# Kernel optimization log

Measured on AMD Instinct MI355X. Metric: run time of the kernel, lower is better.

The kernel has to match this reference:

```python
import jax, jax.numpy as jnp
import numpy as np

NUM_EMBEDDINGS = 512
EMBEDDING_DIM = 64
COMMITMENT_COST = 0.25


def setup_inputs() -> dict:
    key = jax.random.key(0)
    k1, k2 = jax.random.split(key)
    inputs = jax.random.normal(k1, (4, 64, 32, 32, 32), dtype=jnp.float32)
    # torch init: uniform(-1/K, 1/K)
    lim = 1.0 / NUM_EMBEDDINGS
    embedding = jax.random.uniform(k2, (NUM_EMBEDDINGS, EMBEDDING_DIM),
                                   dtype=jnp.float32, minval=-lim, maxval=lim)
    return {"inputs": inputs, "embedding": embedding}


def reference(inputs, embedding):
    # inputs: [B, C, D, H, W] with C == embedding_dim
    x = jnp.transpose(inputs, (0, 2, 3, 4, 1))            # [B,D,H,W,C]
    input_shape = x.shape
    flat = x.reshape(-1, EMBEDDING_DIM)                    # [N,C]
    # squared euclidean distances via matmul expansion
    d = (jnp.sum(flat ** 2, axis=1, keepdims=True)
         + jnp.sum(embedding ** 2, axis=1)
         - 2.0 * flat @ embedding.T)                       # [N,K]
    encoding_indices = jnp.argmin(d, axis=1)               # [N]
    quantized = embedding[encoding_indices].reshape(input_shape)  # [B,D,H,W,C]
    q_latent_loss = jnp.mean((jax.lax.stop_gradient(quantized) - x) ** 2)
    e_latent_loss = jnp.mean((quantized - jax.lax.stop_gradient(x)) ** 2)
    loss = q_latent_loss + COMMITMENT_COST * e_latent_loss
    # straight-through estimator
    quantized = x + jax.lax.stop_gradient(quantized - x)
    quantized = jnp.transpose(quantized, (0, 4, 1, 2, 3))  # [B,C,D,H,W]
    indices = encoding_indices.reshape(input_shape[:-1])   # [B,D,H,W]
    return quantized, loss, indices
```

## Files before the change

kernel.cpp:

```cpp
#include <hip/hip_runtime.h>
#include <math.h>

#define NROWS   131072
#define NCH     64
#define NEMB    512
#define CH_STRIDE 32768
#define B_STRIDE  (64*32768)
#define Q_ELEMS   8388608
#define SPLITS  4
#define KPQ     (NEMB/SPLITS)


__global__ __launch_bounds__(64)
void vq_esq(const float* __restrict__ emb, float* __restrict__ esq) {
    int k = blockIdx.x * 64 + threadIdx.x;
    if (k < NEMB) {
        const float* e = emb + k * NCH;
        float s = 0.f;
        #pragma unroll
        for (int c = 0; c < NCH; ++c) s = fmaf(e[c], e[c], s);
        esq[k] = s;
    }
}

__global__ __launch_bounds__(256, 4)
void vq_scan(const float* __restrict__ in, const float* __restrict__ emb,
             const float* __restrict__ esq,
             unsigned long long* __restrict__ parts) {
    int q      = blockIdx.x & (SPLITS - 1);
    int rowblk = blockIdx.x >> 2;
    int n      = rowblk * 256 + threadIdx.x;
    int b = n >> 15;
    int s = n & 32767;
    const float* xin = in + b * B_STRIDE + s;

    float x[NCH];
    #pragma unroll
    for (int c = 0; c < NCH; ++c) x[c] = xin[c * CH_STRIDE];

    float A;
    {
        float L[16];
        #pragma unroll
        for (int i = 0; i < 16; ++i) {
            float q0 = x[i +  0] * x[i +  0];
            float q1 = x[i + 16] * x[i + 16];
            float q2 = x[i + 32] * x[i + 32];
            float q3 = x[i + 48] * x[i + 48];
            asm volatile("" : "+v"(q0), "+v"(q1), "+v"(q2), "+v"(q3));
            L[i] = (q0 + q1) + (q2 + q3);
        }
        float F[8];
        #pragma unroll
        for (int i = 0; i < 8; ++i) F[i] = L[i] + L[i + 8];
        float G[4];
        #pragma unroll
        for (int i = 0; i < 4; ++i) G[i] = F[i] + F[i + 4];
        A = (G[0] + G[2]) + (G[1] + G[3]);
    }

    int k0 = __builtin_amdgcn_readfirstlane(q * KPQ);
    float m1 = 3.4e38f;
    int   i1 = k0;
    for (int j = 0; j < KPQ; ++j) {
        int k = k0 + j;
        const float* e = emb + k * NCH;
        float acc = 0.f;
        #pragma unroll
        for (int c = 0; c < NCH; ++c) acc = fmaf(x[c], e[c], acc);
        float t1 = A + esq[k];
        float d  = t1 - (acc + acc);
        bool lt = d < m1;
        m1 = lt ? d : m1;
        i1 = lt ? k : i1;
    }

    unsigned long long pk =
        ((unsigned long long)__float_as_uint(m1) << 32) | (unsigned)i1;
    parts[(unsigned)n * SPLITS + q] = pk;
}

__global__ __launch_bounds__(256)
void vq_finish(const float* __restrict__ in, const float* __restrict__ emb,
               const unsigned long long* __restrict__ parts,
               float* __restrict__ out_q, float* __restrict__ out_idx,
               double* __restrict__ loss_acc) {
    int n = blockIdx.x * 256 + threadIdx.x;
    int b = n >> 15;
    int s = n & 32767;

    ulonglong2 pa = *reinterpret_cast<const ulonglong2*>(parts + (unsigned)n * 4);
    ulonglong2 pb = *reinterpret_cast<const ulonglong2*>(parts + (unsigned)n * 4 + 2);
    unsigned long long pk = pa.x;
    if (pa.y < pk) pk = pa.y;
    if (pb.x < pk) pk = pb.x;
    if (pb.y < pk) pk = pb.y;
    int w = (int)(pk & 0xFFFFu);

    const float* xin = in + b * B_STRIDE + s;
    const float* qr  = emb + w * NCH;
    float*       oq  = out_q + b * B_STRIDE + s;
    double rl = 0.0;
    #pragma unroll
    for (int c = 0; c < NCH; c += 4) {
        float4 qv = *reinterpret_cast<const float4*>(qr + c);
        float x0 = xin[(c + 0) * CH_STRIDE];
        float x1 = xin[(c + 1) * CH_STRIDE];
        float x2 = xin[(c + 2) * CH_STRIDE];
        float x3 = xin[(c + 3) * CH_STRIDE];
        oq[(c + 0) * CH_STRIDE] = qv.x;
        oq[(c + 1) * CH_STRIDE] = qv.y;
        oq[(c + 2) * CH_STRIDE] = qv.z;
        oq[(c + 3) * CH_STRIDE] = qv.w;
        double d0 = (double)qv.x - (double)x0;
        double d1 = (double)qv.y - (double)x1;
        double d2 = (double)qv.z - (double)x2;
        double d3 = (double)qv.w - (double)x3;
        rl += d0 * d0 + d1 * d1 + d2 * d2 + d3 * d3;
    }
    out_idx[n] = (float)w;

    #pragma unroll
    for (int off = 32; off; off >>= 1) rl += __shfl_down(rl, off);
    if ((threadIdx.x & 63) == 0) atomicAdd(loss_acc, rl);
}

__global__ void vq_loss_final(const double* __restrict__ loss_acc,
                              float* __restrict__ out_loss) {
    if (threadIdx.x == 0)
        *out_loss = (float)((*loss_acc) * (1.25 / (double)Q_ELEMS));
}

extern "C" void kernel_launch(void* const* d_in, const int* in_sizes, int n_in,
                              void* d_out, int out_size, void* d_ws, size_t ws_size,
                              hipStream_t stream) {
    const float* in  = (const float*)d_in[0];
    const float* emb = (const float*)d_in[1];

    float* out_q    = (float*)d_out;
    float* out_loss = out_q + Q_ELEMS;
    float* out_idx  = out_q + Q_ELEMS + 1;

    char*   ws       = (char*)d_ws;
    double* loss_acc = (double*)ws;
    float*  esq      = (float*)(ws + 16);
    unsigned long long* parts = (unsigned long long*)(ws + 4096);

    hipMemsetAsync(d_ws, 0, 16, stream);
    vq_esq<<<8, 64, 0, stream>>>(emb, esq);
    vq_scan<<<(NROWS / 256) * SPLITS, 256, 0, stream>>>(in, emb, esq, parts);
    vq_finish<<<NROWS / 256, 256, 0, stream>>>(in, emb, parts,
                                               out_q, out_idx, loss_acc);
    vq_loss_final<<<1, 64, 0, stream>>>(loss_acc, out_loss);
}
```

Measured before the change: 263.5 us.

## Stage codebook slice in LDS and transpose partial-argmin layout

```diff
diff --git a/kernel.cpp b/kernel.cpp
--- a/kernel.cpp
+++ b/kernel.cpp
@@ -27,16 +27,31 @@
 void vq_scan(const float* __restrict__ in, const float* __restrict__ emb,
              const float* __restrict__ esq,
              unsigned long long* __restrict__ parts) {
+    __shared__ float4 lds_e[KPQ * 16];
+    __shared__ float  lds_esq[KPQ];
+
     int q      = blockIdx.x & (SPLITS - 1);
     int rowblk = blockIdx.x >> 2;
-    int n      = rowblk * 256 + threadIdx.x;
+    int t      = threadIdx.x;
+    int k0     = q * KPQ;
+    int n      = rowblk * 256 + t;
     int b = n >> 15;
     int s = n & 32767;
     const float* xin = in + b * B_STRIDE + s;
 
+    const float4* gq = reinterpret_cast<const float4*>(emb + k0 * NCH);
+    #pragma unroll
+    for (int i = 0; i < 8; ++i)
+        lds_e[t + i * 256] = gq[t + i * 256];
+    if (t < KPQ) lds_esq[t] = esq[k0 + t];
+
     float x[NCH];
     #pragma unroll
     for (int c = 0; c < NCH; ++c) x[c] = xin[c * CH_STRIDE];
+    #pragma unroll
+    for (int c = 0; c < NCH; c += 8)
+        asm volatile("" : "+v"(x[c]), "+v"(x[c+1]), "+v"(x[c+2]), "+v"(x[c+3]),
+                         "+v"(x[c+4]), "+v"(x[c+5]), "+v"(x[c+6]), "+v"(x[c+7]));
 
     float A;
     {
@@ -59,25 +74,31 @@
         A = (G[0] + G[2]) + (G[1] + G[3]);
     }
 
-    int k0 = __builtin_amdgcn_readfirstlane(q * KPQ);
+    __syncthreads();
+
     float m1 = 3.4e38f;
     int   i1 = k0;
     for (int j = 0; j < KPQ; ++j) {
-        int k = k0 + j;
-        const float* e = emb + k * NCH;
+        const float4* er = lds_e + j * 16;
         float acc = 0.f;
         #pragma unroll
-        for (int c = 0; c < NCH; ++c) acc = fmaf(x[c], e[c], acc);
-        float t1 = A + esq[k];
+        for (int c4 = 0; c4 < 16; ++c4) {
+            float4 ev = er[c4];
+            acc = fmaf(x[c4 * 4 + 0], ev.x, acc);
+            acc = fmaf(x[c4 * 4 + 1], ev.y, acc);
+            acc = fmaf(x[c4 * 4 + 2], ev.z, acc);
+            acc = fmaf(x[c4 * 4 + 3], ev.w, acc);
+        }
+        float t1 = A + lds_esq[j];
         float d  = t1 - (acc + acc);
         bool lt = d < m1;
         m1 = lt ? d : m1;
-        i1 = lt ? k : i1;
+        i1 = lt ? (k0 + j) : i1;
     }
 
     unsigned long long pk =
         ((unsigned long long)__float_as_uint(m1) << 32) | (unsigned)i1;
-    parts[(unsigned)n * SPLITS + q] = pk;
+    parts[(size_t)q * NROWS + n] = pk;
 }
 
 __global__ __launch_bounds__(256)
@@ -89,12 +110,13 @@
     int b = n >> 15;
     int s = n & 32767;
 
-    ulonglong2 pa = *reinterpret_cast<const ulonglong2*>(parts + (unsigned)n * 4);
-    ulonglong2 pb = *reinterpret_cast<const ulonglong2*>(parts + (unsigned)n * 4 + 2);
-    unsigned long long pk = pa.x;
-    if (pa.y < pk) pk = pa.y;
-    if (pb.x < pk) pk = pb.x;
-    if (pb.y < pk) pk = pb.y;
+    unsigned long long pk = parts[n];
+    unsigned long long p1 = parts[(size_t)NROWS + n];
+    unsigned long long p2 = parts[(size_t)2 * NROWS + n];
+    unsigned long long p3 = parts[(size_t)3 * NROWS + n];
+    if (p1 < pk) pk = p1;
+    if (p2 < pk) pk = p2;
+    if (p3 < pk) pk = p3;
     int w = (int)(pk & 0xFFFFu);
 
     const float* xin = in + b * B_STRIDE + s;
```

Measured after the change: 256.5 us. 2.7% less time.
